# Performance work log

Hardware: AMD Instinct MI355X
Metric: run time of the kernel (lower is better)

Reference implementation:

```python
import jax, jax.numpy as jnp
import numpy as np

D, H, DFF, NE, ND, B = 512, 8, 2048, 64, 64, 16

def _ln(x, g, b):
    m = x.mean(-1, keepdims=True)
    v = ((x - m) ** 2).mean(-1, keepdims=True)
    return (x - m) * jax.lax.rsqrt(v + 1e-5) * g + b

def _mha(q, k, v, Wi, bi, Wo, bo, h=H):
    # q,k,v: (L, B, d) seq-first, like torch nn.MultiheadAttention (eval mode)
    Lq, Bb, d = q.shape
    hd = d // h
    Wq, Wk, Wv = jnp.split(Wi, 3, axis=0)
    bq, bk, bv = jnp.split(bi, 3)
    def proj(x, W, bb):
        y = x @ W.T + bb                                  # (L, B, d)
        return y.reshape(x.shape[0], Bb, h, hd).transpose(1, 2, 0, 3)  # (B, h, L, hd)
    qh = proj(q, Wq, bq) * (hd ** -0.5)
    kh = proj(k, Wk, bk)
    vh = proj(v, Wv, bv)
    a = jax.nn.softmax(jnp.einsum('bhqe,bhke->bhqk', qh, kh), axis=-1)
    o = jnp.einsum('bhqk,bhke->bhqe', a, vh).transpose(2, 0, 1, 3).reshape(Lq, Bb, d)
    return o @ Wo.T + bo

def _ffn(x, W1, b1, W2, b2):
    return jax.nn.relu(x @ W1.T + b1) @ W2.T + b2

def _forward(enc, dec, ec_Wi, ec_bi, ec_Wo, ec_bo, dc_Wi, dc_bi, dc_Wo, dc_bo,
             es_Wi, es_bi, es_Wo, es_bo, ds_Wi, ds_bi, ds_Wo, ds_bo,
             eff_W1, eff_b1, eff_W2, eff_b2, dff_W1, dff_b1, dff_W2, dff_b2,
             n_ec_g, n_ec_b, n_es_g, n_es_b, n_ef_g, n_ef_b, n_dc_g, n_dc_b,
             n_dci_g, n_dci_b, n_ds_g, n_ds_b, n_df_g, n_df_b, pW, pWb, pv, pb):
    f_n = _ln(enc, n_ec_g, n_ec_b)   # (ne, B, d) -- normed once, reused for all j
    G_n = _ln(dec, n_dc_g, n_dc_b)   # (nd, B, d)
    # dec_cross for all j at once (key/value is the single token f_j)
    dc_out = jax.vmap(lambda fj: _mha(G_n, fj[None], fj[None], dc_Wi, dc_bi, dc_Wo, dc_bo))(f_n)  # (ne, nd, B, d)
    G_fj = dec[None] + dc_out                            # (ne, nd, B, d)
    G_im = _ln(G_fj, n_dci_g, n_dci_b)
    # enc_cross for all j at once (query is the single token f_j)
    ec_out = jax.vmap(lambda fj, Gj: _mha(fj[None], Gj, Gj, ec_Wi, ec_bi, ec_Wo, ec_bo)[0])(f_n, G_im)  # (ne, B, d)
    enc1 = enc + ec_out
    # attention pooling over the ne fusion copies
    G_c = G_fj.transpose(2, 1, 0, 3)                     # (B, nd, ne, d)
    energy = jnp.tanh(G_c @ pW.T + pWb + pb)
    w = jax.nn.softmax(energy @ pv.T, axis=2)            # (B, nd, ne, 1)
    dec1 = (G_c * w).sum(axis=2).transpose(1, 0, 2)      # (nd, B, d)
    # self-attention + FFN (pre-norm residual)
    en = _ln(enc1, n_es_g, n_es_b)
    enc2 = enc1 + _mha(en, en, en, es_Wi, es_bi, es_Wo, es_bo)
    dn = _ln(dec1, n_ds_g, n_ds_b)
    dec2 = dec1 + _mha(dn, dn, dn, ds_Wi, ds_bi, ds_Wo, ds_bo)
    enc3 = enc2 + _ffn(_ln(enc2, n_ef_g, n_ef_b), eff_W1, eff_b1, eff_W2, eff_b2)
    dec3 = dec2 + _ffn(_ln(dec2, n_df_g, n_df_b), dff_W1, dff_b1, dff_W2, dff_b2)
    return (enc3, dec3)

def setup_inputs() -> dict:
    key = jax.random.key(0)
    ks = iter(jax.random.split(key, 64))
    def w(shape, scale=0.05):
        return jax.random.normal(next(ks), shape, jnp.float32) * scale
    d, dff = D, DFF
    inp = {
        'enc': jax.random.normal(next(ks), (NE, B, d), jnp.float32),
        'dec': jax.random.normal(next(ks), (ND, B, d), jnp.float32),
    }
    for p in ['ec', 'dc', 'es', 'ds']:
        inp[p + '_Wi'] = w((3 * d, d)); inp[p + '_bi'] = jnp.zeros(3 * d, jnp.float32)
        inp[p + '_Wo'] = w((d, d)); inp[p + '_bo'] = jnp.zeros(d, jnp.float32)
    for p in ['eff', 'dff']:
        inp[p + '_W1'] = w((dff, d)); inp[p + '_b1'] = jnp.zeros(dff, jnp.float32)
        inp[p + '_W2'] = w((d, dff)); inp[p + '_b2'] = jnp.zeros(d, jnp.float32)
    for p in ['n_ec', 'n_es', 'n_ef', 'n_dc', 'n_dci', 'n_ds', 'n_df']:
        inp[p + '_g'] = jnp.ones(d, jnp.float32); inp[p + '_b'] = jnp.zeros(d, jnp.float32)
    inp['pW'] = w((d, d)); inp['pWb'] = jnp.zeros(d, jnp.float32)
    inp['pv'] = w((1, d)); inp['pb'] = jnp.zeros(d, jnp.float32)
    return inp

def reference(enc, dec, ec_Wi, ec_bi, ec_Wo, ec_bo, dc_Wi, dc_bi, dc_Wo, dc_bo,
              es_Wi, es_bi, es_Wo, es_bo, ds_Wi, ds_bi, ds_Wo, ds_bo,
              eff_W1, eff_b1, eff_W2, eff_b2, dff_W1, dff_b1, dff_W2, dff_b2,
              n_ec_g, n_ec_b, n_es_g, n_es_b, n_ef_g, n_ef_b, n_dc_g, n_dc_b,
              n_dci_g, n_dci_b, n_ds_g, n_ds_b, n_df_g, n_df_b, pW, pWb, pv, pb):
    return _forward(enc, dec, ec_Wi, ec_bi, ec_Wo, ec_bo, dc_Wi, dc_bi, dc_Wo, dc_bo,
                    es_Wi, es_bi, es_Wo, es_bo, ds_Wi, ds_bi, ds_Wo, ds_bo,
                    eff_W1, eff_b1, eff_W2, eff_b2, dff_W1, dff_b1, dff_W2, dff_b2,
                    n_ec_g, n_ec_b, n_es_g, n_es_b, n_ef_g, n_ef_b, n_dc_g, n_dc_b,
                    n_dci_g, n_dci_b, n_ds_g, n_ds_b, n_df_g, n_df_b, pW, pWb, pv, pb)
```

## Files before the change

### kernel.cpp

```cpp
#include <hip/hip_runtime.h>


typedef __bf16 bf16_t;
typedef bf16_t bf16x8 __attribute__((ext_vector_type(8)));
typedef float f32x4 __attribute__((ext_vector_type(4)));
typedef unsigned short u16x4 __attribute__((ext_vector_type(4)));
typedef unsigned short u16x8 __attribute__((ext_vector_type(8)));

__device__ inline unsigned short f2bf(float f) {
  unsigned int u = __float_as_uint(f);
  u += 0x7fffu + ((u >> 16) & 1u);
  return (unsigned short)(u >> 16);
}
__device__ inline float bf2f(unsigned short u) {
  return __uint_as_float(((unsigned int)u) << 16);
}

__device__ inline float wsum(float v) {
#pragma unroll
  for (int o = 1; o < 64; o <<= 1) v += __shfl_xor(v, o);
  return v;
}
__device__ inline float wmax(float v) {
#pragma unroll
// ... 4 lines not shown
struct CastJob {
  const float* src;
  unsigned short* dst;
  int n;
  const float* cs;
};

__device__ inline void ln_body(const float* __restrict__ x,
                               const float* __restrict__ g,
                               const float* __restrict__ be,
                               unsigned short* __restrict__ y, int t) {
  float v0 = x[t], v1 = x[t + 256];
  float s = wsum(v0 + v1);
  float s2 = wsum(v0 * v0 + v1 * v1);
  __shared__ float sh[8];
  int w = t >> 6, lane = t & 63;
  if (lane == 0) { sh[w] = s; sh[4 + w] = s2; }
  __syncthreads();
  s = sh[0] + sh[1] + sh[2] + sh[3];
  s2 = sh[4] + sh[5] + sh[6] + sh[7];
  float mean = s * (1.f / 512.f);
  float var = s2 * (1.f / 512.f) - mean * mean;
  float r = rsqrtf(var + 1e-5f);
  y[t] = f2bf((v0 - mean) * r * g[t] + be[t]);
  y[t + 256] = f2bf((v1 - mean) * r * g[t + 256] + be[t + 256]);
}

__device__ inline void stats_body(const float* __restrict__ x,
                                  float* __restrict__ m, float* __restrict__ q2,
                                  unsigned short* __restrict__ xb, int t,
                                  int row) {
  float v0 = x[t], v1 = x[t + 256];
  if (xb) {
    xb[t] = f2bf(v0);
    xb[t + 256] = f2bf(v1);
  }
  float s = wsum(v0 + v1);
  float s2 = wsum(v0 * v0 + v1 * v1);
  __shared__ float sh2[8];
  int w = t >> 6, lane = t & 63;
  if (lane == 0) { sh2[w] = s; sh2[4 + w] = s2; }
  __syncthreads();
  if (t == 0) {
    s = sh2[0] + sh2[1] + sh2[2] + sh2[3];
    s2 = sh2[4] + sh2[5] + sh2[6] + sh2[7];
    m[row] = s * (1.f / 512.f);
    q2[row] = s2 * (1.f / 512.f);
  }
}

struct Phase0Args {
  const float* enc; const float* g_ec; const float* b_ec; unsigned short* f_n;
  const float* dec; float* md; float* q2d; unsigned short* dec_b;
  CastJob cast[6];
  const float* Wk; const float* Wv; const float* bk; const float* bv;
  const float* g_dci; const float* b_dci;
  float* u_k; float* u_v; float* c_k; float* c_v;
  float* zbase; int zcount;
};

__global__ __launch_bounds__(256) void phase0(Phase0Args a) {
  int bx = blockIdx.x;
  const int t = threadIdx.x;
  if (bx < 2048) {
    int row = bx;
    if (row < 1024) {
      ln_body(a.enc + (size_t)row * 512, a.g_ec, a.b_ec,
              a.f_n + (size_t)row * 512, t);
    } else {
      row -= 1024;
      stats_body(a.dec + (size_t)row * 512, a.md, a.q2d,
                 a.dec_b + (size_t)row * 512, t, row);
    }
    return;
  }
  bx -= 2048;
  if (bx < 256) {
    const int total = 6 * 262144;
    const int stride = 256 * 256 * 4;
    for (int e = (bx * 256 + t) * 4; e < total; e += stride) {
      int jj = e >> 18;
      int i = e & 262143;
      const CastJob cj = a.cast[jj];
      float4 v = *(const float4*)(cj.src + i);
      if (cj.cs) {
        int k = i & 511;
        v.x *= cj.cs[k]; v.y *= cj.cs[k + 1];
        v.z *= cj.cs[k + 2]; v.w *= cj.cs[k + 3];
      }
      u16x4 o = {f2bf(v.x), f2bf(v.y), f2bf(v.z), f2bf(v.w)};
      *(u16x4*)(cj.dst + i) = o;
    }
    return;
  }
  bx -= 256;
  if (bx < 128) {
    int n = bx * 4 + (t >> 6);
    int lane = t & 63;
    const float* wk = a.Wk + (size_t)n * 512;
    const float* wv = a.Wv + (size_t)n * 512;
    float uk = 0.f, uv = 0.f, ck = 0.f, cv = 0.f;
#pragma unroll
    for (int k0 = 0; k0 < 512; k0 += 64) {
      int k = k0 + lane;
      float x = wk[k], y = wv[k], gg = a.g_dci[k], bb = a.b_dci[k];
      uk += x * gg; ck += x * bb;
      uv += y * gg; cv += y * bb;
    }
    uk = wsum(uk); uv = wsum(uv); ck = wsum(ck); cv = wsum(cv);
    if (lane == 0) {
      a.u_k[n] = uk; a.u_v[n] = uv;
      a.c_k[n] = ck + a.bk[n]; a.c_v[n] = cv + a.bv[n];
    }
    return;
  }
  for (int i = t; i < a.zcount; i += 256) a.zbase[i] = 0.f;
}

struct GemmJob {
  const unsigned short* X;
  const float* Xf;
  const float* Asum; const float* Asq;
  const float* g; const float* be;
  const unsigned short* W;
  const float* bias;
  const float* resid;
  float* Y;
  unsigned short* Ybf;
  float* Ssum; float* Ssq;
  float scale;
  int relu;
};
struct MrJob {
  const unsigned short* A; const unsigned short* B;
  const float* md; const float* q2d;
  const float* ts; const float* tsq;
  float* mArr; float* rArr;
};
struct PoolJob {
  const float* Ed; const float* Et; const float* pv; const float* dec;
  const unsigned short* tbf; float* dec1; float* d1s; float* d1q;
};
struct GemmBatch {
  GemmJob j[5];
  MrJob mr;
  CastJob c[9];
  PoolJob pl;
};

__device__ inline u16x8 fold_pack(float4 va, float4 vb, const float* gp,
                                  const float* bp, float m, float ri) {
  float4 g0 = *(const float4*)gp;
  float4 g1 = *(const float4*)(gp + 4);
  float4 e0 = *(const float4*)bp;
  float4 e1 = *(const float4*)(bp + 4);
  u16x8 o;
  o[0] = f2bf((va.x - m) * ri * g0.x + e0.x);
  o[1] = f2bf((va.y - m) * ri * g0.y + e0.y);
  o[2] = f2bf((va.z - m) * ri * g0.z + e0.z);
  o[3] = f2bf((va.w - m) * ri * g0.w + e0.w);
  o[4] = f2bf((vb.x - m) * ri * g1.x + e1.x);
  o[5] = f2bf((vb.y - m) * ri * g1.y + e1.y);
  o[6] = f2bf((vb.z - m) * ri * g1.z + e1.z);
  o[7] = f2bf((vb.w - m) * ri * g1.w + e1.w);
  return o;
// ... 197 lines not shown
      if constexpr (FOLD) {
        const float* p0 = jb.Xf + (size_t)(bm + r0) * K + kn + o0;
        const float* p1 = jb.Xf + (size_t)(bm + r1) * K + kn + o1;
        fa0a = *(const float4*)p0; fa0b = *(const float4*)(p0 + 4);
        fa1a = *(const float4*)p1; fa1b = *(const float4*)(p1 + 4);
      } else {
        xa0 = *(const u16x8*)&Xp[(size_t)r0 * K + kn + o0];
        xa1 = *(const u16x8*)&Xp[(size_t)r1 * K + kn + o1];
      }
      wa0 = *(const u16x8*)&Wp[(size_t)r0 * K + kn + o0];
      wa1 = *(const u16x8*)&Wp[(size_t)r1 * K + kn + o1];
    }
#pragma unroll
    for (int ks = 0; ks < 2; ++ks) {
      int kk = ks * 32 + fg * 8;
      bf16x8 a0 = *(const bf16x8*)&As[wr * 32 + fr][kk];
      bf16x8 a1 = *(const bf16x8*)&As[wr * 32 + 16 + fr][kk];
      bf16x8 b0 = *(const bf16x8*)&Bs[wc * 32 + fr][kk];
      bf16x8 b1 = *(const bf16x8*)&Bs[wc * 32 + 16 + fr][kk];
      acc[0][0] = __builtin_amdgcn_mfma_f32_16x16x32_bf16(a0, b0, acc[0][0], 0, 0, 0);
      acc[0][1] = __builtin_amdgcn_mfma_f32_16x16x32_bf16(a0, b1, acc[0][1], 0, 0, 0);
      acc[1][0] = __builtin_amdgcn_mfma_f32_16x16x32_bf16(a1, b0, acc[1][0], 0, 0, 0);
      acc[1][1] = __builtin_amdgcn_mfma_f32_16x16x32_bf16(a1, b1, acc[1][1], 0, 0, 0);
    }
    __syncthreads();
  }
  float rsum[2][4], rsq[2][4];
  if constexpr (STATS) {
#pragma unroll
    for (int mt = 0; mt < 2; ++mt)
#pragma unroll
      for (int r = 0; r < 4; ++r) { rsum[mt][r] = 0.f; rsq[mt][r] = 0.f; }
  }
#pragma unroll
  for (int mt = 0; mt < 2; ++mt) {
#pragma unroll
    for (int nt = 0; nt < 2; ++nt) {
      int col = bn + wc * 32 + nt * 16 + fr;
      int rowb = bm + wr * 32 + mt * 16 + fg * 4;
      float bia = jb.bias ? jb.bias[col] : 0.f;
#pragma unroll
      for (int r = 0; r < 4; ++r) {
        float v = (acc[mt][nt][r] + bia) * jb.scale;
        if (jb.relu) v = fmaxf(v, 0.f);
        if (jb.resid) v += jb.resid[(size_t)(rowb + r) * N + col];
        size_t idx = (size_t)(rowb + r) * N + col;
        if (jb.Y) jb.Y[idx] = v;
        if (jb.Ybf) jb.Ybf[idx] = f2bf(v);
        if constexpr (STATS) { rsum[mt][r] += v; rsq[mt][r] += v * v; }
      }
    }
  }
  if constexpr (STATS) {
#pragma unroll
    for (int mt = 0; mt < 2; ++mt)
#pragma unroll
      for (int r = 0; r < 4; ++r) {
        float s = rsum[mt][r], q = rsq[mt][r];
#pragma unroll
        for (int o = 1; o < 16; o <<= 1) {
          s += __shfl_xor(s, o);
          q += __shfl_xor(q, o);
        }
        if (fr == 0) {
          int row = bm + wr * 32 + mt * 16 + fg * 4 + r;
          atomicAdd(&jb.Ssum[row], s);
          atomicAdd(&jb.Ssq[row], q);
        }
      }
  }
}

__global__ __launch_bounds__(256) void ec_attn(
    const unsigned short* __restrict__ Qe, const unsigned short* __restrict__ Kd,
    const unsigned short* __restrict__ Kt, const unsigned short* __restrict__ Vd,
    const unsigned short* __restrict__ Vt, const float* __restrict__ u_k,
    const float* __restrict__ u_v, const float* __restrict__ c_k,
    const float* __restrict__ c_v, const float* __restrict__ mArr,
    const float* __restrict__ rArr, unsigned short* __restrict__ O) {
  int h = blockIdx.x & 7;
  int b = blockIdx.x >> 3;
  __shared__ unsigned short Qs[64][72];
  __shared__ unsigned short Ks[64][72];
  __shared__ unsigned short VdT[64][72];
  __shared__ unsigned short Ps[64][72];
  __shared__ float ms[64][66];
  __shared__ float rs[64][66];
  __shared__ float stp[64][4], sup[64][4], scp[64][4];
  __shared__ float stv[64], suv[64], scv[64], swv[64], swmv[64];
  int t = threadIdx.x;
  {
    int row = t >> 2;
    int qt = t & 3;
    int cb = qt * 16;
    size_t base = (size_t)(row * 16 + b) * 512 + h * 64 + cb;
    u16x8 q0 = *(const u16x8*)(Qe + base);
    u16x8 q1 = *(const u16x8*)(Qe + base + 8);
    u16x8 k0 = *(const u16x8*)(Kd + base);
    u16x8 k1 = *(const u16x8*)(Kd + base + 8);
    u16x8 kt0 = *(const u16x8*)(Kt + base);
    u16x8 kt1 = *(const u16x8*)(Kt + base + 8);
    u16x8 v0 = *(const u16x8*)(Vd + base);
    u16x8 v1 = *(const u16x8*)(Vd + base + 8);
    *(u16x8*)&Qs[row][cb] = q0;
    *(u16x8*)&Qs[row][cb + 8] = q1;
    *(u16x8*)&Ks[row][cb] = k0;
    *(u16x8*)&Ks[row][cb + 8] = k1;
#pragma unroll
    for (int jj = 0; jj < 8; ++jj) VdT[cb + jj][row] = v0[jj];
#pragma unroll
    for (int jj = 0; jj < 8; ++jj) VdT[cb + 8 + jj][row] = v1[jj];
    float st_ = 0.f, su_ = 0.f, sc_ = 0.f;
#pragma unroll
    for (int jj = 0; jj < 8; ++jj) {
      float qa = bf2f(q0[jj]), qb = bf2f(q1[jj]);
      st_ += qa * bf2f(kt0[jj]) + qb * bf2f(kt1[jj]);
      su_ += qa * u_k[h * 64 + cb + jj] + qb * u_k[h * 64 + cb + 8 + jj];
      sc_ += qa * c_k[h * 64 + cb + jj] + qb * c_k[h * 64 + cb + 8 + jj];
    }
    stp[row][qt] = st_;
    sup[row][qt] = su_;
    scp[row][qt] = sc_;
  }
#pragma unroll
  for (int k = 0; k < 16; ++k) {
    int idx = t + k * 256;
    ms[idx >> 6][idx & 63] = mArr[(size_t)b * 4096 + idx];
    rs[idx >> 6][idx & 63] = rArr[(size_t)b * 4096 + idx];
  }
  __syncthreads();
  if (t < 64) {
    stv[t] = stp[t][0] + stp[t][1] + stp[t][2] + stp[t][3];
    suv[t] = sup[t][0] + sup[t][1] + sup[t][2] + sup[t][3];
    scv[t] = scp[t][0] + scp[t][1] + scp[t][2] + scp[t][3];
  }
  __syncthreads();
  int wave = t >> 6, lane = t & 63;
  int fr = lane & 15, fg = lane >> 4;
  f32x4 sacc[4] = {};
  bf16x8 aq0 = *(const bf16x8*)&Qs[wave * 16 + fr][fg * 8];
  bf16x8 aq1 = *(const bf16x8*)&Qs[wave * 16 + fr][32 + fg * 8];
#pragma unroll
  for (int nt = 0; nt < 4; ++nt) {
    bf16x8 b0 = *(const bf16x8*)&Ks[nt * 16 + fr][fg * 8];
    bf16x8 b1 = *(const bf16x8*)&Ks[nt * 16 + fr][32 + fg * 8];
    sacc[nt] = __builtin_amdgcn_mfma_f32_16x16x32_bf16(aq0, b0, sacc[nt], 0, 0, 0);
    sacc[nt] = __builtin_amdgcn_mfma_f32_16x16x32_bf16(aq1, b1, sacc[nt], 0, 0, 0);
  }
#pragma unroll
  for (int r = 0; r < 4; ++r) {
    int j = wave * 16 + fg * 4 + r;
    float stj = stv[j], suj = suv[j], scj = scv[j];
    float a0, a1, a2, a3;
    {
      int i0 = fr, i1 = 16 + fr, i2 = 32 + fr, i3 = 48 + fr;
      a0 = rs[j][i0] * (sacc[0][r] + stj - ms[j][i0] * suj) + scj;
      a1 = rs[j][i1] * (sacc[1][r] + stj - ms[j][i1] * suj) + scj;
      a2 = rs[j][i2] * (sacc[2][r] + stj - ms[j][i2] * suj) + scj;
      a3 = rs[j][i3] * (sacc[3][r] + stj - ms[j][i3] * suj) + scj;
    }
    float mx = fmaxf(fmaxf(a0, a1), fmaxf(a2, a3));
#pragma unroll
    for (int o = 1; o < 16; o <<= 1) mx = fmaxf(mx, __shfl_xor(mx, o));
    a0 = __expf(a0 - mx);
    a1 = __expf(a1 - mx);
    a2 = __expf(a2 - mx);
    a3 = __expf(a3 - mx);
    float se = a0 + a1 + a2 + a3;
#pragma unroll
    for (int o = 1; o < 16; o <<= 1) se += __shfl_xor(se, o);
    float inv = 1.f / se;
    float w0 = a0 * inv * rs[j][fr];
    float w1 = a1 * inv * rs[j][16 + fr];
    float w2 = a2 * inv * rs[j][32 + fr];
    float w3 = a3 * inv * rs[j][48 + fr];
    float sw = w0 + w1 + w2 + w3;
    float swm = w0 * ms[j][fr] + w1 * ms[j][16 + fr] + w2 * ms[j][32 + fr] +
                w3 * ms[j][48 + fr];
#pragma unroll
    for (int o = 1; o < 16; o <<= 1) {
      sw += __shfl_xor(sw, o);
      swm += __shfl_xor(swm, o);
    }
    Ps[j][fr] = f2bf(w0);
    Ps[j][16 + fr] = f2bf(w1);
    Ps[j][32 + fr] = f2bf(w2);
    Ps[j][48 + fr] = f2bf(w3);
    if (fr == 0) {
      swv[j] = sw;
      swmv[j] = swm;
    }
  }
  f32x4 oc[4] = {};
  bf16x8 ap0 = *(const bf16x8*)&Ps[wave * 16 + fr][fg * 8];
  bf16x8 ap1 = *(const bf16x8*)&Ps[wave * 16 + fr][32 + fg * 8];
#pragma unroll
  for (int nt = 0; nt < 4; ++nt) {
    bf16x8 b0 = *(const bf16x8*)&VdT[nt * 16 + fr][fg * 8];
    bf16x8 b1 = *(const bf16x8*)&VdT[nt * 16 + fr][32 + fg * 8];
    oc[nt] = __builtin_amdgcn_mfma_f32_16x16x32_bf16(ap0, b0, oc[nt], 0, 0, 0);
    oc[nt] = __builtin_amdgcn_mfma_f32_16x16x32_bf16(ap1, b1, oc[nt], 0, 0, 0);
  }
#pragma unroll
  for (int nt = 0; nt < 4; ++nt) {
    int d = nt * 16 + fr;
    float uvd = u_v[h * 64 + d];
    float cvd = c_v[h * 64 + d];
#pragma unroll
    for (int r = 0; r < 4; ++r) {
      int j = wave * 16 + fg * 4 + r;
      size_t gidx = (size_t)(j * 16 + b) * 512 + h * 64 + d;
      float o = oc[nt][r] + swv[j] * bf2f(Vt[gidx]) - swmv[j] * uvd + cvd;
      O[gidx] = f2bf(o);
    }
  }
}

__global__ __launch_bounds__(256) void self_attn(
    const unsigned short* __restrict__ QKVe, unsigned short* __restrict__ Oe,
    const unsigned short* __restrict__ QKVd, unsigned short* __restrict__ Od) {
  const unsigned short* QKV = blockIdx.y ? QKVd : QKVe;
  unsigned short* O = blockIdx.y ? Od : Oe;
  int h = blockIdx.x & 7;
  int b = blockIdx.x >> 3;
  __shared__ unsigned short Qs[64][72];
  __shared__ unsigned short Ksh[64][72];
  __shared__ unsigned short VT[64][72];
  __shared__ unsigned short Ps[64][72];
  int t = threadIdx.x;
  {
    int row = t >> 2;
    int cb = (t & 3) * 16;
    const unsigned short* src =
        QKV + (size_t)(row * 16 + b) * 1536 + h * 64 + cb;
    u16x8 q0 = *(const u16x8*)(src);
    u16x8 q1 = *(const u16x8*)(src + 8);
    u16x8 k0 = *(const u16x8*)(src + 512);
    u16x8 k1 = *(const u16x8*)(src + 520);
    u16x8 v0 = *(const u16x8*)(src + 1024);
    u16x8 v1 = *(const u16x8*)(src + 1032);
    *(u16x8*)&Qs[row][cb] = q0;
    *(u16x8*)&Qs[row][cb + 8] = q1;
    *(u16x8*)&Ksh[row][cb] = k0;
    *(u16x8*)&Ksh[row][cb + 8] = k1;
#pragma unroll
    for (int jj = 0; jj < 8; ++jj) VT[cb + jj][row] = v0[jj];
#pragma unroll
    for (int jj = 0; jj < 8; ++jj) VT[cb + 8 + jj][row] = v1[jj];
  }
  __syncthreads();
  int wave = t >> 6, lane = t & 63;
  int fr = lane & 15, fg = lane >> 4;
  f32x4 sc[4] = {};
  bf16x8 aq0 = *(const bf16x8*)&Qs[wave * 16 + fr][fg * 8];
  bf16x8 aq1 = *(const bf16x8*)&Qs[wave * 16 + fr][32 + fg * 8];
#pragma unroll
  for (int nt = 0; nt < 4; ++nt) {
    bf16x8 b0 = *(const bf16x8*)&Ksh[nt * 16 + fr][fg * 8];
    bf16x8 b1 = *(const bf16x8*)&Ksh[nt * 16 + fr][32 + fg * 8];
    sc[nt] = __builtin_amdgcn_mfma_f32_16x16x32_bf16(aq0, b0, sc[nt], 0, 0, 0);
    sc[nt] = __builtin_amdgcn_mfma_f32_16x16x32_bf16(aq1, b1, sc[nt], 0, 0, 0);
  }
#pragma unroll
  for (int r = 0; r < 4; ++r) {
    float a0 = sc[0][r] * 0.125f, a1 = sc[1][r] * 0.125f;
    float a2 = sc[2][r] * 0.125f, a3 = sc[3][r] * 0.125f;
    float mx = fmaxf(fmaxf(a0, a1), fmaxf(a2, a3));
#pragma unroll
    for (int o = 1; o < 16; o <<= 1) mx = fmaxf(mx, __shfl_xor(mx, o));
    a0 = __expf(a0 - mx);
    a1 = __expf(a1 - mx);
    a2 = __expf(a2 - mx);
    a3 = __expf(a3 - mx);
    float se = a0 + a1 + a2 + a3;
#pragma unroll
    for (int o = 1; o < 16; o <<= 1) se += __shfl_xor(se, o);
    float inv = 1.f / se;
    int prow = wave * 16 + fg * 4 + r;
    Ps[prow][0 + fr] = f2bf(a0 * inv);
    Ps[prow][16 + fr] = f2bf(a1 * inv);
    Ps[prow][32 + fr] = f2bf(a2 * inv);
    Ps[prow][48 + fr] = f2bf(a3 * inv);
  }
  f32x4 oc[4] = {};
  bf16x8 ap0 = *(const bf16x8*)&Ps[wave * 16 + fr][fg * 8];
  bf16x8 ap1 = *(const bf16x8*)&Ps[wave * 16 + fr][32 + fg * 8];
#pragma unroll
  for (int nt = 0; nt < 4; ++nt) {
    bf16x8 b0 = *(const bf16x8*)&VT[nt * 16 + fr][fg * 8];
    bf16x8 b1 = *(const bf16x8*)&VT[nt * 16 + fr][32 + fg * 8];
    oc[nt] = __builtin_amdgcn_mfma_f32_16x16x32_bf16(ap0, b0, oc[nt], 0, 0, 0);
    oc[nt] = __builtin_amdgcn_mfma_f32_16x16x32_bf16(ap1, b1, oc[nt], 0, 0, 0);
  }
#pragma unroll
  for (int nt = 0; nt < 4; ++nt) {
#pragma unroll
    for (int r = 0; r < 4; ++r) {
      int q = wave * 16 + fg * 4 + r;
      int d = nt * 16 + fr;
      O[(size_t)(q * 16 + b) * 512 + h * 64 + d] = f2bf(oc[nt][r]);
    }
  }
}

extern "C" void kernel_launch(void* const* d_in, const int* in_sizes, int n_in,
                              void* d_out, int out_size, void* d_ws,
                              size_t ws_size, hipStream_t stream) {
  const float* enc = (const float*)d_in[0];
  const float* dec = (const float*)d_in[1];
  const float* ec_Wi = (const float*)d_in[2];
  const float* ec_bi = (const float*)d_in[3];
  const float* ec_Wo = (const float*)d_in[4];
  const float* ec_bo = (const float*)d_in[5];
  const float* dc_Wi = (const float*)d_in[6];
  const float* dc_bi = (const float*)d_in[7];
  const float* dc_Wo = (const float*)d_in[8];
  const float* dc_bo = (const float*)d_in[9];
  const float* es_Wi = (const float*)d_in[10];
  const float* es_bi = (const float*)d_in[11];
  const float* es_Wo = (const float*)d_in[12];
  const float* es_bo = (const float*)d_in[13];
  const float* ds_Wi = (const float*)d_in[14];
  const float* ds_bi = (const float*)d_in[15];
  const float* ds_Wo = (const float*)d_in[16];
  const float* ds_bo = (const float*)d_in[17];
  const float* eff_W1 = (const float*)d_in[18];
  const float* eff_b1 = (const float*)d_in[19];
  const float* eff_W2 = (const float*)d_in[20];
  const float* eff_b2 = (const float*)d_in[21];
  const float* dff_W1 = (const float*)d_in[22];
  const float* dff_b1 = (const float*)d_in[23];
  const float* dff_W2 = (const float*)d_in[24];
  const float* dff_b2 = (const float*)d_in[25];
  const float* n_ec_g = (const float*)d_in[26];
  const float* n_ec_b = (const float*)d_in[27];
  const float* n_es_g = (const float*)d_in[28];
  const float* n_es_b = (const float*)d_in[29];
  const float* n_ef_g = (const float*)d_in[30];
  const float* n_ef_b = (const float*)d_in[31];
  const float* n_dci_g = (const float*)d_in[34];
  const float* n_dci_b = (const float*)d_in[35];
  const float* n_ds_g = (const float*)d_in[36];
  const float* n_ds_b = (const float*)d_in[37];
  const float* n_df_g = (const float*)d_in[38];
  const float* n_df_b = (const float*)d_in[39];
  const float* pW = (const float*)d_in[40];
  const float* pWb = (const float*)d_in[41];
  const float* pv = (const float*)d_in[42];
  const float* pb = (const float*)d_in[43];

  float* ws = (float*)d_ws;
  const size_t U = 524288;
  float* Ed = ws + 3 * U;
  float* Et = ws + 7 * U;
  float* enc1 = ws + 8 * U;
  float* dec1 = ws + 9 * U;
  float* enc2 = ws + 10 * U;
  float* dec2 = ws + 11 * U;
  float* sm = ws + 12 * U;
  float* md = sm;
  float* q2d = sm + 1024;
  float* u_k = sm + 4096;
  float* u_v = sm + 4608;
  float* c_k = sm + 5120;
  float* c_v = sm + 5632;
  float* mArr = sm + 6144;
  float* rArr = sm + 6144 + 65536;
  float* stx = ws + 24 * U;
  float* t_s = stx;
  float* t_sq = stx + 1024;
  float* e1s = stx + 2048;
  float* e1q = stx + 3072;
  float* d1s = stx + 4096;
  float* d1q = stx + 5120;
  float* e2s = stx + 6144;
  float* e2q = stx + 7168;
  float* d2s = stx + 8192;
  float* d2q = stx + 9216;
  unsigned short* ub0 = (unsigned short*)ws;
  unsigned short* Qe_b = ub0 + 0 * U;
  unsigned short* Kd_b = ub0 + 1 * U;
  unsigned short* Vd_b = ub0 + 2 * U;
  unsigned short* Kt_b = ub0 + 3 * U;
  unsigned short* Vt_b = ub0 + 4 * U;
  unsigned short* ub = (unsigned short*)(ws + 12 * U + 137216);
  const int W262 = 262144, W786 = 786432, W1M = 1048576;
  unsigned short* w_dcWv = ub;
  unsigned short* w_ecWq = w_dcWv + W262;
  unsigned short* w_ecWkg = w_ecWq + W262;
  unsigned short* w_ecWvg = w_ecWkg + W262;
  unsigned short* w_pW = w_ecWvg + W262;
  unsigned short* w_dcWo = w_pW + W262;
  unsigned short* w_ecWo = w_dcWo + W262;
  unsigned short* w_esWi = w_ecWo + W262;
  unsigned short* w_dsWi = w_esWi + W786;
  unsigned short* w_esWo = w_dsWi + W786;
  unsigned short* w_dsWo = w_esWo + W262;
  unsigned short* w_effW1 = w_dsWo + W262;
  unsigned short* w_dffW1 = w_effW1 + W1M;
  unsigned short* w_effW2 = w_dffW1 + W1M;
  unsigned short* w_dffW2 = w_effW2 + W1M;
  unsigned short* actb = w_dffW2 + W1M;
  unsigned short* f_n_b = actb;
  unsigned short* V1_b = actb + U;
  unsigned short* dec_b = actb + 2 * U;
  unsigned short* tb_b = actb + 3 * U;
  unsigned short* Oec_b = actb + 4 * U;
  unsigned short* OaE = dec_b;
  unsigned short* OaD = tb_b;
  unsigned short* QKVe_b = (unsigned short*)(ws + 0 * U);
  unsigned short* QKVd_b = (unsigned short*)(ws + 2 * U);
  unsigned short* He_b = (unsigned short*)(ws + 0 * U);
  unsigned short* Hd_b = (unsigned short*)(ws + 2 * U);

  const float* dc_Wv = dc_Wi + 1024 * 512;
  const float* dc_bv = dc_bi + 1024;
  const float* ec_Wq = ec_Wi;
  const float* ec_bq = ec_bi;
  const float* ec_Wk = ec_Wi + 512 * 512;
  const float* ec_bk = ec_bi + 512;
  const float* ec_Wv = ec_Wi + 1024 * 512;
  const float* ec_bv = ec_bi + 1024;

  auto J = [](const unsigned short* X, const unsigned short* W,
              const float* bias, const float* resid, float* Y,
              unsigned short* Ybf, float scale, int relu) {
    GemmJob j{};
    j.X = X; j.W = W; j.bias = bias; j.resid = resid;
    j.Y = Y; j.Ybf = Ybf; j.scale = scale; j.relu = relu;
    return j;
  };
  auto JF = [](const float* Xf, const float* As, const float* Aq,
               const float* g, const float* be, const unsigned short* W,
               const float* bias, unsigned short* Ybf, int relu) {
    GemmJob j{};
    j.Xf = Xf; j.Asum = As; j.Asq = Aq; j.g = g; j.be = be;
    j.W = W; j.bias = bias; j.Ybf = Ybf; j.scale = 1.f; j.relu = relu;
    return j;
  };

  {
    Phase0Args pa{};
    pa.enc = enc; pa.g_ec = n_ec_g; pa.b_ec = n_ec_b; pa.f_n = f_n_b;
    pa.dec = dec; pa.md = md; pa.q2d = q2d; pa.dec_b = dec_b;
    pa.cast[0] = {dc_Wv, w_dcWv, W262, nullptr};
    pa.cast[1] = {ec_Wq, w_ecWq, W262, nullptr};
    pa.cast[2] = {ec_Wk, w_ecWkg, W262, n_dci_g};
    pa.cast[3] = {ec_Wv, w_ecWvg, W262, n_dci_g};
    pa.cast[4] = {pW, w_pW, W262, nullptr};
    pa.cast[5] = {dc_Wo, w_dcWo, W262, nullptr};
    pa.Wk = ec_Wk; pa.Wv = ec_Wv; pa.bk = ec_bk; pa.bv = ec_bv;
    pa.g_dci = n_dci_g; pa.b_dci = n_dci_b;
    pa.u_k = u_k; pa.u_v = u_v; pa.c_k = c_k; pa.c_v = c_v;
    pa.zbase = stx; pa.zcount = 10240;
    phase0<<<2433, 256, 0, stream>>>(pa);
  }
  {
    GemmBatch gb{};
    gb.j[0] = J(f_n_b, w_dcWv, dc_bv, nullptr, nullptr, V1_b, 1.f, 0);
    gb.j[1] = J(f_n_b, w_ecWq, ec_bq, nullptr, nullptr, Qe_b, 0.125f, 0);
    gb.j[2] = J(dec_b, w_ecWkg, nullptr, nullptr, nullptr, Kd_b, 1.f, 0);
    gb.j[3] = J(dec_b, w_ecWvg, nullptr, nullptr, nullptr, Vd_b, 1.f, 0);
    gb.j[4] = J(dec_b, w_pW, pWb, nullptr, Ed, nullptr, 1.f, 0);
    gb.c[0] = {ec_Wo, w_ecWo, W262, nullptr};
    gb.c[1] = {es_Wi, w_esWi, W786, nullptr};
    gb.c[2] = {ds_Wi, w_dsWi, W786, nullptr};
    gb.c[3] = {es_Wo, w_esWo, W262, nullptr};
    gb.c[4] = {ds_Wo, w_dsWo, W262, nullptr};
    gb.c[5] = {eff_W1, w_effW1, W1M, nullptr};
    gb.c[6] = {dff_W1, w_dffW1, W1M, nullptr};
    gb.c[7] = {eff_W2, w_effW2, W1M, nullptr};
    gb.c[8] = {dff_W2, w_dffW2, W1M, nullptr};
    gemm_bf16<1, false, false><<<dim3(8, 16, 6), 256, 0, stream>>>(
        gb, 1024, 512, 512, 5);
  }
  {
    GemmBatch gb{};
    gb.j[0] = J(V1_b, w_dcWo, dc_bo, nullptr, nullptr, tb_b, 1.f, 0);
    gb.j[0].Ssum = t_s; gb.j[0].Ssq = t_sq;
    gemm_bf16<0, false, true><<<dim3(8, 16, 1), 256, 0, stream>>>(
        gb, 1024, 512, 512, -1);
  }
  {
    GemmBatch gb{};
    gb.j[0] = J(tb_b, w_ecWkg, nullptr, nullptr, nullptr, Kt_b, 1.f, 0);
    gb.j[1] = J(tb_b, w_ecWvg, nullptr, nullptr, nullptr, Vt_b, 1.f, 0);
    gb.j[2] = J(tb_b, w_pW, pb, nullptr, Et, nullptr, 1.f, 0);
    gb.mr = {dec_b, tb_b, md, q2d, t_s, t_sq, mArr, rArr};
    gemm_bf16<2, false, false><<<dim3(8, 16, 4), 256, 0, stream>>>(
        gb, 1024, 512, 512, 3);
  }
  ec_attn<<<128, 256, 0, stream>>>(Qe_b, Kd_b, Kt_b, Vd_b, Vt_b, u_k, u_v, c_k,
                                   c_v, mArr, rArr, Oec_b);
  {
    GemmBatch gb{};
    gb.j[0] = J(Oec_b, w_ecWo, ec_bo, enc, enc1, nullptr, 1.f, 0);
    gb.j[0].Ssum = e1s; gb.j[0].Ssq = e1q;
    gb.pl = {Ed, Et, pv, dec, tb_b, dec1, d1s, d1q};
    gemm_bf16<3, false, true><<<dim3(8, 16, 9), 256, 0, stream>>>(
        gb, 1024, 512, 512, 1);
  }
  {
    GemmBatch gb{};
    gb.j[0] = JF(enc1, e1s, e1q, n_es_g, n_es_b, w_esWi, es_bi, QKVe_b, 0);
    gb.j[1] = JF(dec1, d1s, d1q, n_ds_g, n_ds_b, w_dsWi, ds_bi, QKVd_b, 0);
    gemm_bf16<0, true, false><<<dim3(24, 16, 2), 256, 0, stream>>>(
        gb, 1024, 1536, 512, -1);
  }
  self_attn<<<dim3(128, 2), 256, 0, stream>>>(QKVe_b, OaE, QKVd_b, OaD);
  {
    GemmBatch gb{};
    gb.j[0] = J(OaE, w_esWo, es_bo, enc1, enc2, nullptr, 1.f, 0);
    gb.j[0].Ssum = e2s; gb.j[0].Ssq = e2q;
    gb.j[1] = J(OaD, w_dsWo, ds_bo, dec1, dec2, nullptr, 1.f, 0);
    gb.j[1].Ssum = d2s; gb.j[1].Ssq = d2q;
    gemm_bf16<0, false, true><<<dim3(8, 16, 2), 256, 0, stream>>>(
        gb, 1024, 512, 512, -1);
  }
  {
    GemmBatch gb{};
    gb.j[0] = JF(enc2, e2s, e2q, n_ef_g, n_ef_b, w_effW1, eff_b1, He_b, 1);
    gb.j[1] = JF(dec2, d2s, d2q, n_df_g, n_df_b, w_dffW1, dff_b1, Hd_b, 1);
    gemm_bf16<0, true, false><<<dim3(32, 16, 2), 256, 0, stream>>>(
        gb, 1024, 2048, 512, -1);
  }
  float* out = (float*)d_out;
  {
    GemmBatch gb{};
    gb.j[0] = J(He_b, w_effW2, eff_b2, enc2, out, nullptr, 1.f, 0);
    gb.j[1] = J(Hd_b, w_dffW2, dff_b2, dec2, out + U, nullptr, 1.f, 0);
    gemm_bf16<0, false, false><<<dim3(8, 16, 2), 256, 0, stream>>>(
        gb, 1024, 512, 2048, -1);
  }
}
```

Measured before the change: 310.3 us.

## Fold dec-cross V and output projections into one weight; split attention blocks by query

Precomputes Wf = dc_Wo·dc_Wv in bf16 with MFMA inside phase0, plus the fused bias Wo·bv+bo. The cross-attention value path then becomes a single GEMM over the normalized encoder rows, which removes one GEMM launch and the V1 intermediate round trip. The row statistics move into the batched GEMM epilogue, which is now guarded by a null check on Ssum. ec_attn and self_attn are also split into two 32-query blocks of 128 threads each, doubling the grid, with m/r read directly from global memory. Costs: an extra rounding step from the bf16 product weight, and K/V tiles are loaded twice per head.

```diff
diff --git a/kernel.cpp b/kernel.cpp
--- a/kernel.cpp
+++ b/kernel.cpp
@@ -80,16 +80,83 @@
 struct Phase0Args {
   const float* enc; const float* g_ec; const float* b_ec; unsigned short* f_n;
   const float* dec; float* md; float* q2d; unsigned short* dec_b;
-  CastJob cast[6];
+  CastJob cast[4];
   const float* Wk; const float* Wv; const float* bk; const float* bv;
   const float* g_dci; const float* b_dci;
   float* u_k; float* u_v; float* c_k; float* c_v;
+  const float* WoA; const float* WvA; unsigned short* Wfb;
+  const float* bv2; const float* bo2; float* bf_out;
   float* zbase; int zcount;
 };
 
 __global__ __launch_bounds__(256) void phase0(Phase0Args a) {
+  __shared__ unsigned short WAs[64][72];
+  __shared__ unsigned short WBs[64][72];
   int bx = blockIdx.x;
   const int t = threadIdx.x;
+  if (bx < 64) {
+    const int bm = (bx >> 3) * 64;
+    const int bn = (bx & 7) * 64;
+    const int lane = t & 63;
+    const int wave = t >> 6;
+    const int wr = wave >> 1;
+    const int wc = wave & 1;
+    const int fr = lane & 15;
+    const int fg = lane >> 4;
+    const int rr = t >> 2;
+    const int c = (t & 3) * 16;
+    f32x4 acc[2][2] = {};
+    for (int m0 = 0; m0 < 512; m0 += 64) {
+      const float* ap = a.WoA + (size_t)(bm + rr) * 512 + m0 + c;
+      float4 a0 = *(const float4*)ap;
+      float4 a1 = *(const float4*)(ap + 4);
+      float4 a2 = *(const float4*)(ap + 8);
+      float4 a3 = *(const float4*)(ap + 12);
+      u16x8 lo = {f2bf(a0.x), f2bf(a0.y), f2bf(a0.z), f2bf(a0.w),
+                  f2bf(a1.x), f2bf(a1.y), f2bf(a1.z), f2bf(a1.w)};
+      u16x8 hi = {f2bf(a2.x), f2bf(a2.y), f2bf(a2.z), f2bf(a2.w),
+                  f2bf(a3.x), f2bf(a3.y), f2bf(a3.z), f2bf(a3.w)};
+      *(u16x8*)&WAs[rr][c] = lo;
+      *(u16x8*)&WAs[rr][c + 8] = hi;
+      const float* bp = a.WvA + (size_t)(m0 + rr) * 512 + bn + c;
+      float4 b0 = *(const float4*)bp;
+      float4 b1 = *(const float4*)(bp + 4);
+      float4 b2 = *(const float4*)(bp + 8);
+      float4 b3 = *(const float4*)(bp + 12);
+      float bv16[16] = {b0.x, b0.y, b0.z, b0.w, b1.x, b1.y, b1.z, b1.w,
+                        b2.x, b2.y, b2.z, b2.w, b3.x, b3.y, b3.z, b3.w};
+#pragma unroll
+      for (int jj = 0; jj < 16; ++jj) WBs[c + jj][rr] = f2bf(bv16[jj]);
+      __syncthreads();
+#pragma unroll
+      for (int ks = 0; ks < 2; ++ks) {
+        int kk = ks * 32 + fg * 8;
+        bf16x8 fa0 = *(const bf16x8*)&WAs[wr * 32 + fr][kk];
+        bf16x8 fa1 = *(const bf16x8*)&WAs[wr * 32 + 16 + fr][kk];
+        bf16x8 fb0 = *(const bf16x8*)&WBs[wc * 32 + fr][kk];
+        bf16x8 fb1 = *(const bf16x8*)&WBs[wc * 32 + 16 + fr][kk];
+        acc[0][0] = __builtin_amdgcn_mfma_f32_16x16x32_bf16(fa0, fb0, acc[0][0], 0, 0, 0);
+        acc[0][1] = __builtin_amdgcn_mfma_f32_16x16x32_bf16(fa0, fb1, acc[0][1], 0, 0, 0);
+        acc[1][0] = __builtin_amdgcn_mfma_f32_16x16x32_bf16(fa1, fb0, acc[1][0], 0, 0, 0);
+        acc[1][1] = __builtin_amdgcn_mfma_f32_16x16x32_bf16(fa1, fb1, acc[1][1], 0, 0, 0);
+      }
+      __syncthreads();
+    }
+#pragma unroll
+    for (int mt = 0; mt < 2; ++mt) {
+#pragma unroll
+      for (int nt = 0; nt < 2; ++nt) {
+        int col = bn + wc * 32 + nt * 16 + fr;
+        int rowb = bm + wr * 32 + mt * 16 + fg * 4;
+#pragma unroll
+        for (int r = 0; r < 4; ++r) {
+          a.Wfb[(size_t)(rowb + r) * 512 + col] = f2bf(acc[mt][nt][r]);
+        }
+      }
+    }
+    return;
+  }
+  bx -= 64;
   if (bx < 2048) {
     int row = bx;
     if (row < 1024) {
@@ -104,7 +171,7 @@
   }
   bx -= 2048;
   if (bx < 256) {
-    const int total = 6 * 262144;
+    const int total = 4 * 262144;
     const int stride = 256 * 256 * 4;
     for (int e = (bx * 256 + t) * 4; e < total; e += stride) {
       int jj = e >> 18;
@@ -127,18 +194,22 @@
     int lane = t & 63;
     const float* wk = a.Wk + (size_t)n * 512;
     const float* wv = a.Wv + (size_t)n * 512;
-    float uk = 0.f, uv = 0.f, ck = 0.f, cv = 0.f;
+    const float* wo = a.WoA + (size_t)n * 512;
+    float uk = 0.f, uv = 0.f, ck = 0.f, cv = 0.f, bfa = 0.f;
 #pragma unroll
     for (int k0 = 0; k0 < 512; k0 += 64) {
       int k = k0 + lane;
       float x = wk[k], y = wv[k], gg = a.g_dci[k], bb = a.b_dci[k];
       uk += x * gg; ck += x * bb;
       uv += y * gg; cv += y * bb;
+      bfa += wo[k] * a.bv2[k];
     }
     uk = wsum(uk); uv = wsum(uv); ck = wsum(ck); cv = wsum(cv);
+    bfa = wsum(bfa);
     if (lane == 0) {
       a.u_k[n] = uk; a.u_v[n] = uv;
       a.c_k[n] = ck + a.bk[n]; a.c_v[n] = cv + a.bv[n];
+      a.bf_out[n] = bfa + a.bo2[n];
     }
     return;
   }
@@ -442,64 +513,56 @@
     }
   }
   if constexpr (STATS) {
-#pragma unroll
-    for (int mt = 0; mt < 2; ++mt)
-#pragma unroll
-      for (int r = 0; r < 4; ++r) {
-        float s = rsum[mt][r], q = rsq[mt][r];
-#pragma unroll
-        for (int o = 1; o < 16; o <<= 1) {
-          s += __shfl_xor(s, o);
-          q += __shfl_xor(q, o);
+    if (jb.Ssum) {
+#pragma unroll
+      for (int mt = 0; mt < 2; ++mt)
+#pragma unroll
+        for (int r = 0; r < 4; ++r) {
+          float s = rsum[mt][r], q = rsq[mt][r];
+#pragma unroll
+          for (int o = 1; o < 16; o <<= 1) {
+            s += __shfl_xor(s, o);
+            q += __shfl_xor(q, o);
+          }
+          if (fr == 0) {
+            int row = bm + wr * 32 + mt * 16 + fg * 4 + r;
+            atomicAdd(&jb.Ssum[row], s);
+            atomicAdd(&jb.Ssq[row], q);
+          }
         }
-        if (fr == 0) {
-          int row = bm + wr * 32 + mt * 16 + fg * 4 + r;
-          atomicAdd(&jb.Ssum[row], s);
-          atomicAdd(&jb.Ssq[row], q);
-        }
-      }
-  }
-}
-
-__global__ __launch_bounds__(256) void ec_attn(
+    }
+  }
+}
+
+__global__ __launch_bounds__(128) void ec_attn(
     const unsigned short* __restrict__ Qe, const unsigned short* __restrict__ Kd,
     const unsigned short* __restrict__ Kt, const unsigned short* __restrict__ Vd,
     const unsigned short* __restrict__ Vt, const float* __restrict__ u_k,
     const float* __restrict__ u_v, const float* __restrict__ c_k,
     const float* __restrict__ c_v, const float* __restrict__ mArr,
     const float* __restrict__ rArr, unsigned short* __restrict__ O) {
-  int h = blockIdx.x & 7;
-  int b = blockIdx.x >> 3;
-  __shared__ unsigned short Qs[64][72];
+  int bx = blockIdx.x;
+  int h = bx & 7;
+  int b = (bx >> 3) & 15;
+  int jlo = (bx >> 7) * 32;
+  __shared__ unsigned short Qs[32][72];
   __shared__ unsigned short Ks[64][72];
   __shared__ unsigned short VdT[64][72];
-  __shared__ unsigned short Ps[64][72];
-  __shared__ float ms[64][66];
-  __shared__ float rs[64][66];
-  __shared__ float stp[64][4], sup[64][4], scp[64][4];
-  __shared__ float stv[64], suv[64], scv[64], swv[64], swmv[64];
+  __shared__ unsigned short Ps[32][72];
+  __shared__ float stp[32][4], sup[32][4], scp[32][4];
+  __shared__ float stv[32], suv[32], scv[32], swv[32], swmv[32];
   int t = threadIdx.x;
   {
     int row = t >> 2;
     int qt = t & 3;
     int cb = qt * 16;
-    size_t base = (size_t)(row * 16 + b) * 512 + h * 64 + cb;
+    size_t base = (size_t)((jlo + row) * 16 + b) * 512 + h * 64 + cb;
     u16x8 q0 = *(const u16x8*)(Qe + base);
     u16x8 q1 = *(const u16x8*)(Qe + base + 8);
-    u16x8 k0 = *(const u16x8*)(Kd + base);
-    u16x8 k1 = *(const u16x8*)(Kd + base + 8);
     u16x8 kt0 = *(const u16x8*)(Kt + base);
     u16x8 kt1 = *(const u16x8*)(Kt + base + 8);
-    u16x8 v0 = *(const u16x8*)(Vd + base);
-    u16x8 v1 = *(const u16x8*)(Vd + base + 8);
     *(u16x8*)&Qs[row][cb] = q0;
     *(u16x8*)&Qs[row][cb + 8] = q1;
-    *(u16x8*)&Ks[row][cb] = k0;
-    *(u16x8*)&Ks[row][cb + 8] = k1;
-#pragma unroll
-    for (int jj = 0; jj < 8; ++jj) VdT[cb + jj][row] = v0[jj];
-#pragma unroll
-    for (int jj = 0; jj < 8; ++jj) VdT[cb + 8 + jj][row] = v1[jj];
     float st_ = 0.f, su_ = 0.f, sc_ = 0.f;
 #pragma unroll
     for (int jj = 0; jj < 8; ++jj) {
@@ -511,15 +574,32 @@
     stp[row][qt] = st_;
     sup[row][qt] = su_;
     scp[row][qt] = sc_;
-  }
-#pragma unroll
-  for (int k = 0; k < 16; ++k) {
-    int idx = t + k * 256;
-    ms[idx >> 6][idx & 63] = mArr[(size_t)b * 4096 + idx];
-    rs[idx >> 6][idx & 63] = rArr[(size_t)b * 4096 + idx];
+    int row2 = t >> 1;
+    int c0 = (t & 1) * 32;
+    size_t base2 = (size_t)(row2 * 16 + b) * 512 + h * 64 + c0;
+    u16x8 k0 = *(const u16x8*)(Kd + base2);
+    u16x8 k1 = *(const u16x8*)(Kd + base2 + 8);
+    u16x8 k2 = *(const u16x8*)(Kd + base2 + 16);
+    u16x8 k3 = *(const u16x8*)(Kd + base2 + 24);
+    u16x8 v0 = *(const u16x8*)(Vd + base2);
+    u16x8 v1 = *(const u16x8*)(Vd + base2 + 8);
+    u16x8 v2 = *(const u16x8*)(Vd + base2 + 16);
+    u16x8 v3 = *(const u16x8*)(Vd + base2 + 24);
+    *(u16x8*)&Ks[row2][c0] = k0;
+    *(u16x8*)&Ks[row2][c0 + 8] = k1;
+    *(u16x8*)&Ks[row2][c0 + 16] = k2;
+    *(u16x8*)&Ks[row2][c0 + 24] = k3;
+#pragma unroll
+    for (int jj = 0; jj < 8; ++jj) VdT[c0 + jj][row2] = v0[jj];
+#pragma unroll
+    for (int jj = 0; jj < 8; ++jj) VdT[c0 + 8 + jj][row2] = v1[jj];
+#pragma unroll
+    for (int jj = 0; jj < 8; ++jj) VdT[c0 + 16 + jj][row2] = v2[jj];
+#pragma unroll
+    for (int jj = 0; jj < 8; ++jj) VdT[c0 + 24 + jj][row2] = v3[jj];
   }
   __syncthreads();
-  if (t < 64) {
+  if (t < 32) {
     stv[t] = stp[t][0] + stp[t][1] + stp[t][2] + stp[t][3];
     suv[t] = sup[t][0] + sup[t][1] + sup[t][2] + sup[t][3];
     scv[t] = scp[t][0] + scp[t][1] + scp[t][2] + scp[t][3];
@@ -539,16 +619,17 @@
   }
 #pragma unroll
   for (int r = 0; r < 4; ++r) {
-    int j = wave * 16 + fg * 4 + r;
-    float stj = stv[j], suj = suv[j], scj = scv[j];
-    float a0, a1, a2, a3;
-    {
-      int i0 = fr, i1 = 16 + fr, i2 = 32 + fr, i3 = 48 + fr;
-      a0 = rs[j][i0] * (sacc[0][r] + stj - ms[j][i0] * suj) + scj;
-      a1 = rs[j][i1] * (sacc[1][r] + stj - ms[j][i1] * suj) + scj;
-      a2 = rs[j][i2] * (sacc[2][r] + stj - ms[j][i2] * suj) + scj;
-      a3 = rs[j][i3] * (sacc[3][r] + stj - ms[j][i3] * suj) + scj;
-    }
+    int lj = wave * 16 + fg * 4 + r;
+    int gj = jlo + lj;
+    const float* mrow = mArr + (size_t)b * 4096 + gj * 64;
+    const float* rrow = rArr + (size_t)b * 4096 + gj * 64;
+    float m0 = mrow[fr], m1 = mrow[16 + fr], m2 = mrow[32 + fr], m3 = mrow[48 + fr];
+    float r0v = rrow[fr], r1v = rrow[16 + fr], r2v = rrow[32 + fr], r3v = rrow[48 + fr];
+    float stj = stv[lj], suj = suv[lj], scj = scv[lj];
+    float a0 = r0v * (sacc[0][r] + stj - m0 * suj) + scj;
+    float a1 = r1v * (sacc[1][r] + stj - m1 * suj) + scj;
+    float a2 = r2v * (sacc[2][r] + stj - m2 * suj) + scj;
+    float a3 = r3v * (sacc[3][r] + stj - m3 * suj) + scj;
     float mx = fmaxf(fmaxf(a0, a1), fmaxf(a2, a3));
 #pragma unroll
     for (int o = 1; o < 16; o <<= 1) mx = fmaxf(mx, __shfl_xor(mx, o));
@@ -560,25 +641,24 @@
 #pragma unroll
     for (int o = 1; o < 16; o <<= 1) se += __shfl_xor(se, o);
     float inv = 1.f / se;
-    float w0 = a0 * inv * rs[j][fr];
-    float w1 = a1 * inv * rs[j][16 + fr];
-    float w2 = a2 * inv * rs[j][32 + fr];
-    float w3 = a3 * inv * rs[j][48 + fr];
+    float w0 = a0 * inv * r0v;
+    float w1 = a1 * inv * r1v;
+    float w2 = a2 * inv * r2v;
+    float w3 = a3 * inv * r3v;
     float sw = w0 + w1 + w2 + w3;
-    float swm = w0 * ms[j][fr] + w1 * ms[j][16 + fr] + w2 * ms[j][32 + fr] +
-                w3 * ms[j][48 + fr];
+    float swm = w0 * m0 + w1 * m1 + w2 * m2 + w3 * m3;
 #pragma unroll
     for (int o = 1; o < 16; o <<= 1) {
       sw += __shfl_xor(sw, o);
       swm += __shfl_xor(swm, o);
     }
-    Ps[j][fr] = f2bf(w0);
-    Ps[j][16 + fr] = f2bf(w1);
-    Ps[j][32 + fr] = f2bf(w2);
-    Ps[j][48 + fr] = f2bf(w3);
+    Ps[lj][fr] = f2bf(w0);
+    Ps[lj][16 + fr] = f2bf(w1);
+    Ps[lj][32 + fr] = f2bf(w2);
+    Ps[lj][48 + fr] = f2bf(w3);
     if (fr == 0) {
-      swv[j] = sw;
-      swmv[j] = swm;
+      swv[lj] = sw;
+      swmv[lj] = swm;
     }
   }
   f32x4 oc[4] = {};
@@ -598,45 +678,61 @@
     float cvd = c_v[h * 64 + d];
 #pragma unroll
     for (int r = 0; r < 4; ++r) {
-      int j = wave * 16 + fg * 4 + r;
-      size_t gidx = (size_t)(j * 16 + b) * 512 + h * 64 + d;
-      float o = oc[nt][r] + swv[j] * bf2f(Vt[gidx]) - swmv[j] * uvd + cvd;
+      int lj = wave * 16 + fg * 4 + r;
+      int gj = jlo + lj;
+      size_t gidx = (size_t)(gj * 16 + b) * 512 + h * 64 + d;
+      float o = oc[nt][r] + swv[lj] * bf2f(Vt[gidx]) - swmv[lj] * uvd + cvd;
       O[gidx] = f2bf(o);
     }
   }
 }
 
-__global__ __launch_bounds__(256) void self_attn(
+__global__ __launch_bounds__(128) void self_attn(
     const unsigned short* __restrict__ QKVe, unsigned short* __restrict__ Oe,
     const unsigned short* __restrict__ QKVd, unsigned short* __restrict__ Od) {
-  const unsigned short* QKV = blockIdx.y ? QKVd : QKVe;
-  unsigned short* O = blockIdx.y ? Od : Oe;
+  const unsigned short* QKV = blockIdx.z ? QKVd : QKVe;
+  unsigned short* O = blockIdx.z ? Od : Oe;
   int h = blockIdx.x & 7;
   int b = blockIdx.x >> 3;
-  __shared__ unsigned short Qs[64][72];
+  int qlo = blockIdx.y * 32;
+  __shared__ unsigned short Qs[32][72];
   __shared__ unsigned short Ksh[64][72];
   __shared__ unsigned short VT[64][72];
-  __shared__ unsigned short Ps[64][72];
+  __shared__ unsigned short Ps[32][72];
   int t = threadIdx.x;
   {
     int row = t >> 2;
     int cb = (t & 3) * 16;
     const unsigned short* src =
-        QKV + (size_t)(row * 16 + b) * 1536 + h * 64 + cb;
+        QKV + (size_t)((qlo + row) * 16 + b) * 1536 + h * 64 + cb;
     u16x8 q0 = *(const u16x8*)(src);
     u16x8 q1 = *(const u16x8*)(src + 8);
-    u16x8 k0 = *(const u16x8*)(src + 512);
-    u16x8 k1 = *(const u16x8*)(src + 520);
-    u16x8 v0 = *(const u16x8*)(src + 1024);
-    u16x8 v1 = *(const u16x8*)(src + 1032);
     *(u16x8*)&Qs[row][cb] = q0;
     *(u16x8*)&Qs[row][cb + 8] = q1;
-    *(u16x8*)&Ksh[row][cb] = k0;
-    *(u16x8*)&Ksh[row][cb + 8] = k1;
-#pragma unroll
-    for (int jj = 0; jj < 8; ++jj) VT[cb + jj][row] = v0[jj];
-#pragma unroll
-    for (int jj = 0; jj < 8; ++jj) VT[cb + 8 + jj][row] = v1[jj];
+    int row2 = t >> 1;
+    int c0 = (t & 1) * 32;
+    const unsigned short* src2 =
+        QKV + (size_t)(row2 * 16 + b) * 1536 + h * 64 + c0;
+    u16x8 k0 = *(const u16x8*)(src2 + 512);
+    u16x8 k1 = *(const u16x8*)(src2 + 520);
+    u16x8 k2 = *(const u16x8*)(src2 + 528);
+    u16x8 k3 = *(const u16x8*)(src2 + 536);
+    u16x8 v0 = *(const u16x8*)(src2 + 1024);
+    u16x8 v1 = *(const u16x8*)(src2 + 1032);
+    u16x8 v2 = *(const u16x8*)(src2 + 1040);
+    u16x8 v3 = *(const u16x8*)(src2 + 1048);
+    *(u16x8*)&Ksh[row2][c0] = k0;
+    *(u16x8*)&Ksh[row2][c0 + 8] = k1;
+    *(u16x8*)&Ksh[row2][c0 + 16] = k2;
+    *(u16x8*)&Ksh[row2][c0 + 24] = k3;
+#pragma unroll
+    for (int jj = 0; jj < 8; ++jj) VT[c0 + jj][row2] = v0[jj];
+#pragma unroll
+    for (int jj = 0; jj < 8; ++jj) VT[c0 + 8 + jj][row2] = v1[jj];
+#pragma unroll
+    for (int jj = 0; jj < 8; ++jj) VT[c0 + 16 + jj][row2] = v2[jj];
+#pragma unroll
+    for (int jj = 0; jj < 8; ++jj) VT[c0 + 24 + jj][row2] = v3[jj];
   }
   __syncthreads();
   int wave = t >> 6, lane = t & 63;
@@ -686,7 +782,7 @@
   for (int nt = 0; nt < 4; ++nt) {
 #pragma unroll
     for (int r = 0; r < 4; ++r) {
-      int q = wave * 16 + fg * 4 + r;
+      int q = qlo + wave * 16 + fg * 4 + r;
       int d = nt * 16 + fr;
       O[(size_t)(q * 16 + b) * 512 + h * 64 + d] = f2bf(oc[nt][r]);
     }
@@ -750,6 +846,7 @@
   float* sm = ws + 12 * U;
   float* md = sm;
   float* q2d = sm + 1024;
+  float* bf = sm + 2048;
   float* u_k = sm + 4096;
   float* u_v = sm + 4608;
   float* c_k = sm + 5120;
@@ -775,13 +872,13 @@
   unsigned short* Vt_b = ub0 + 4 * U;
   unsigned short* ub = (unsigned short*)(ws + 12 * U + 137216);
   const int W262 = 262144, W786 = 786432, W1M = 1048576;
-  unsigned short* w_dcWv = ub;
-  unsigned short* w_ecWq = w_dcWv + W262;
+  unsigned short* w_Wf = ub;
+  unsigned short* w_ecWq = w_Wf + W262;
   unsigned short* w_ecWkg = w_ecWq + W262;
   unsigned short* w_ecWvg = w_ecWkg + W262;
   unsigned short* w_pW = w_ecWvg + W262;
-  unsigned short* w_dcWo = w_pW + W262;
-  unsigned short* w_ecWo = w_dcWo + W262;
+  unsigned short* w_unused = w_pW + W262;
+  unsigned short* w_ecWo = w_unused + W262;
   unsigned short* w_esWi = w_ecWo + W262;
   unsigned short* w_dsWi = w_esWi + W786;
   unsigned short* w_esWo = w_dsWi + W786;
@@ -792,7 +889,6 @@
   unsigned short* w_dffW2 = w_effW2 + W1M;
   unsigned short* actb = w_dffW2 + W1M;
   unsigned short* f_n_b = actb;
-  unsigned short* V1_b = actb + U;
   unsigned short* dec_b = actb + 2 * U;
   unsigned short* tb_b = actb + 3 * U;
   unsigned short* Oec_b = actb + 4 * U;
@@ -833,21 +929,22 @@
     Phase0Args pa{};
     pa.enc = enc; pa.g_ec = n_ec_g; pa.b_ec = n_ec_b; pa.f_n = f_n_b;
     pa.dec = dec; pa.md = md; pa.q2d = q2d; pa.dec_b = dec_b;
-    pa.cast[0] = {dc_Wv, w_dcWv, W262, nullptr};
-    pa.cast[1] = {ec_Wq, w_ecWq, W262, nullptr};
-    pa.cast[2] = {ec_Wk, w_ecWkg, W262, n_dci_g};
-    pa.cast[3] = {ec_Wv, w_ecWvg, W262, n_dci_g};
-    pa.cast[4] = {pW, w_pW, W262, nullptr};
-    pa.cast[5] = {dc_Wo, w_dcWo, W262, nullptr};
+    pa.cast[0] = {ec_Wq, w_ecWq, W262, nullptr};
+    pa.cast[1] = {ec_Wk, w_ecWkg, W262, n_dci_g};
+    pa.cast[2] = {ec_Wv, w_ecWvg, W262, n_dci_g};
+    pa.cast[3] = {pW, w_pW, W262, nullptr};
     pa.Wk = ec_Wk; pa.Wv = ec_Wv; pa.bk = ec_bk; pa.bv = ec_bv;
     pa.g_dci = n_dci_g; pa.b_dci = n_dci_b;
     pa.u_k = u_k; pa.u_v = u_v; pa.c_k = c_k; pa.c_v = c_v;
+    pa.WoA = dc_Wo; pa.WvA = dc_Wv; pa.Wfb = w_Wf;
+    pa.bv2 = dc_bv; pa.bo2 = dc_bo; pa.bf_out = bf;
     pa.zbase = stx; pa.zcount = 10240;
-    phase0<<<2433, 256, 0, stream>>>(pa);
+    phase0<<<2497, 256, 0, stream>>>(pa);
   }
   {
     GemmBatch gb{};
-    gb.j[0] = J(f_n_b, w_dcWv, dc_bv, nullptr, nullptr, V1_b, 1.f, 0);
+    gb.j[0] = J(f_n_b, w_Wf, bf, nullptr, nullptr, tb_b, 1.f, 0);
+    gb.j[0].Ssum = t_s; gb.j[0].Ssq = t_sq;
     gb.j[1] = J(f_n_b, w_ecWq, ec_bq, nullptr, nullptr, Qe_b, 0.125f, 0);
     gb.j[2] = J(dec_b, w_ecWkg, nullptr, nullptr, nullptr, Kd_b, 1.f, 0);
     gb.j[3] = J(dec_b, w_ecWvg, nullptr, nullptr, nullptr, Vd_b, 1.f, 0);
@@ -861,15 +958,8 @@
     gb.c[6] = {dff_W1, w_dffW1, W1M, nullptr};
     gb.c[7] = {eff_W2, w_effW2, W1M, nullptr};
     gb.c[8] = {dff_W2, w_dffW2, W1M, nullptr};
-    gemm_bf16<1, false, false><<<dim3(8, 16, 6), 256, 0, stream>>>(
+    gemm_bf16<1, false, true><<<dim3(8, 16, 6), 256, 0, stream>>>(
         gb, 1024, 512, 512, 5);
-  }
-  {
-    GemmBatch gb{};
-    gb.j[0] = J(V1_b, w_dcWo, dc_bo, nullptr, nullptr, tb_b, 1.f, 0);
-    gb.j[0].Ssum = t_s; gb.j[0].Ssq = t_sq;
-    gemm_bf16<0, false, true><<<dim3(8, 16, 1), 256, 0, stream>>>(
-        gb, 1024, 512, 512, -1);
   }
   {
     GemmBatch gb{};
@@ -880,7 +970,7 @@
     gemm_bf16<2, false, false><<<dim3(8, 16, 4), 256, 0, stream>>>(
         gb, 1024, 512, 512, 3);
   }
-  ec_attn<<<128, 256, 0, stream>>>(Qe_b, Kd_b, Kt_b, Vd_b, Vt_b, u_k, u_v, c_k,
+  ec_attn<<<256, 128, 0, stream>>>(Qe_b, Kd_b, Kt_b, Vd_b, Vt_b, u_k, u_v, c_k,
                                    c_v, mArr, rArr, Oec_b);
   {
     GemmBatch gb{};
@@ -897,7 +987,7 @@
     gemm_bf16<0, true, false><<<dim3(24, 16, 2), 256, 0, stream>>>(
         gb, 1024, 1536, 512, -1);
   }
-  self_attn<<<dim3(128, 2), 256, 0, stream>>>(QKVe_b, OaE, QKVd_b, OaD);
+  self_attn<<<dim3(128, 2, 2), 128, 0, stream>>>(QKVe_b, OaE, QKVd_b, OaD);
   {
     GemmBatch gb{};
     gb.j[0] = J(OaE, w_esWo, es_bo, enc1, enc2, nullptr, 1.f, 0);
```

After: 297.9 us. 4.0% less time.
